# Optimization experiments

Measured on AMD Instinct MI355X. Metric: run time of the kernel, lower is better.

The kernel has to match this reference:

```python
import jax, jax.numpy as jnp
import numpy as np

B, M, T, L, K = 64, 16, 2048, 64, 32
N = T - L + 1  # 1985 sliding-window positions


def setup_inputs() -> dict:
    key = jax.random.key(0)
    k1, k2, k3 = jax.random.split(key, 3)
    x = jax.random.normal(k1, (B, M, T), dtype=jnp.float32)
    # shapelets initialized uniform(-1, 1) as in nn.init.uniform_
    shapelets = jax.random.uniform(k2, (K, L), dtype=jnp.float32, minval=-1.0, maxval=1.0)
    # penalty maps (learned; zeros at init, random here for a non-trivial weighting)
    penalty_maps = 0.1 * jax.random.normal(k3, (K, M, N), dtype=jnp.float32)
    return {"x": x, "shapelets": shapelets, "penalty_maps": penalty_maps}


def reference(x, shapelets, penalty_maps):
    # x: (B, M, T); shapelets: (K, L); penalty_maps: (K, M, N)
    Lw = shapelets.shape[1]
    n_pos = x.shape[2] - Lw + 1
    # sliding-window view: (B, M, N, L), equivalent to torch unfold(dim=2, size=L, step=1)
    idx = jnp.arange(n_pos)[:, None] + jnp.arange(Lw)[None, :]
    sub = x[:, :, idx]  # (B, M, N, L)

    def per_shapelet(args):
        shp, pmap = args  # (L,), (M, N)
        # raw squared L2 distance over window, per channel/position: (B, M, N)
        raw = jnp.sum((sub - shp[None, None, None, :]) ** 2, axis=3)
        pen = jax.nn.elu(-pmap) + 2.0  # (M, N)
        wd = jnp.sum(raw * pen[None], axis=1)  # sum over channels -> (B, N)
        return jnp.min(wd, axis=1)  # min over positions -> (B,)

    # sequential map over the K shapelets avoids a Kx blow-up of the (B,M,N,L) intermediate
    feats = jax.lax.map(per_shapelet, (shapelets, penalty_maps))  # (K, B)
    return feats.T  # (B, K)
```

## Files before the change

### kernel.cpp

```cpp
#include <hip/hip_runtime.h>
#include <hip/hip_bf16.h>

#define B_ 64
#define M_ 16
#define T_ 2048
#define L_ 64
#define K_ 32
#define N_ (T_ - L_ + 1)
#define TN 64
#define NT_ 32
#define NTH 256
#define XROW 144
#define STSTR 72
#define PENK (NT_ * M_ * 64)
#define PENSZ (K_ * PENK)

typedef __attribute__((ext_vector_type(8))) short bf16x8;
typedef __attribute__((ext_vector_type(4))) float f32x4;

__device__ __forceinline__ unsigned short f2bf(float f) {
    __hip_bfloat16 h = __float2bfloat16(f);
    return __builtin_bit_cast(unsigned short, h);
}

__device__ __forceinline__ float elu_pen(float p) {
    return (p < 0.f) ? (2.f - p) : (__expf(-p) + 1.f);
}

__global__ void pen_init_kernel(const float* __restrict__ pmap,
                                const float* __restrict__ shp,
                                float* __restrict__ pen,
                                float* __restrict__ ss_ws,
                                unsigned* __restrict__ out) {
    const int gid = blockIdx.x * 256 + threadIdx.x;
    if (gid < B_ * K_) out[gid] = 0x7F800000u;
    if (gid < K_) {
        float s = 0.f;
        for (int l = 0; l < L_; ++l) { float v = shp[gid * L_ + l]; s = fmaf(v, v, s); }
        ss_ws[gid] = s;
    }
    if (gid < PENSZ / 4) {
        const int o = gid * 4;
        const int nin = o & 63;
        const int m   = (o >> 6) & 15;
        const int nt  = (o >> 10) & 31;
        const int k   = o >> 15;
        const int n   = nt * TN + nin;
        const float* src = pmap + ((size_t)k * M_ + m) * N_ + n;
        float p[4];
        if (n + 3 < N_) {
            float4 v = *(const float4*)src;
            p[0] = v.x; p[1] = v.y; p[2] = v.z; p[3] = v.w;
        } else {
#pragma unroll
            for (int i = 0; i < 4; ++i) p[i] = (n + i < N_) ? src[i] : 0.f;
        }
        float4 r;
        r.x = elu_pen(p[0]); r.y = elu_pen(p[1]);
        r.z = elu_pen(p[2]); r.w = elu_pen(p[3]);
        *(float4*)(pen + o) = r;
    }
}

__global__ __launch_bounds__(NTH, 4)
void shapelet_mfma_kernel(const float* __restrict__ x,
                          const float* __restrict__ shp,
                          const float* __restrict__ pen,
                          const float* __restrict__ ss_ws,
                          unsigned* __restrict__ out) {
    __shared__ __align__(16) unsigned short xbuf4[M_][4][XROW];
    __shared__ __align__(16) unsigned short st[K_][STSTR];
    __shared__ __align__(16) float sqw[M_][TN];

    const int tid = threadIdx.x;
    const int bx = blockIdx.x;
    const int n0 = bx * TN;
    const int b  = blockIdx.y;
    const bool fast = (n0 + 2 * TN <= T_);

    const int lane = tid & 63;
    const int w  = tid >> 6;
    const int rl = lane & 15;
    const int q  = lane >> 4;
    const int sp = rl & 3;
    const int e0 = 16 * w + 8 * q + (rl & ~3);
    const int eq = e0 >> 2;
    const int nrow = n0 + 16 * w + 4 * q;

    const float ssk0 = ss_ws[rl], ssk1 = ss_ws[16 + rl];

    const float* pb0 = pen + (size_t)rl * PENK + (size_t)bx * (M_ * 64) + (16 * w + 4 * q);
    const float* pb1 = pb0 + (size_t)16 * PENK;

    float4 pa0 = *(const float4*)(pb0);
    float4 pa1 = *(const float4*)(pb1);
    float4 pc0 = *(const float4*)(pb0 + 64);
    float4 pc1 = *(const float4*)(pb1 + 64);

    if (tid < 128) {
        const int m = tid >> 3, j0 = (tid & 7) * 8;
        const float* xr = x + ((size_t)b * M_ + m) * T_ + n0;
        float s = 0.f;
        if (fast) {
#pragma unroll
            for (int qd = 0; qd < 16; ++qd) {
                float4 v = *(const float4*)(xr + j0 + qd * 4);
                s = fmaf(v.x, v.x, s); s = fmaf(v.y, v.y, s);
                s = fmaf(v.z, v.z, s); s = fmaf(v.w, v.w, s);
            }
            sqw[m][j0] = s;
#pragma unroll
            for (int d = 1; d < 8; ++d) {
                float a = xr[j0 + d + L_ - 1], r = xr[j0 + d - 1];
                s += a * a - r * r;
                sqw[m][j0 + d] = s;
            }
        } else {
            for (int l = 0; l < L_; ++l) {
                float v = (n0 + j0 + l < T_) ? xr[j0 + l] : 0.f;
                s = fmaf(v, v, s);
            }
            sqw[m][j0] = s;
            for (int d = 1; d < 8; ++d) {
                float a = (n0 + j0 + d + L_ - 1 < T_) ? xr[j0 + d + L_ - 1] : 0.f;
                float r = (n0 + j0 + d - 1 < T_) ? xr[j0 + d - 1] : 0.f;
                s += a * a - r * r;
                sqw[m][j0 + d] = s;
            }
        }
    } else {
        const int t2 = tid - 128;
        const float* xb = x + ((size_t)b * M_) * T_ + n0;
        for (int g = t2; g < M_ * 31; g += 128) {
            const int m = g / 31, j4 = (g - m * 31) * 4;
            const float* src = xb + m * T_ + j4;
            float h[8];
            if (fast) {
                float4 v0 = *(const float4*)src;
                float4 v1 = *(const float4*)(src + 4);
                h[0] = v0.x; h[1] = v0.y; h[2] = v0.z; h[3] = v0.w;
                h[4] = v1.x; h[5] = v1.y; h[6] = v1.z; h[7] = v1.w;
            } else {
#pragma unroll
                for (int i = 0; i < 8; ++i)
                    h[i] = (n0 + j4 + i < T_) ? src[i] : 0.f;
            }
            unsigned short hb[8];
#pragma unroll
            for (int i = 0; i < 8; ++i) hb[i] = f2bf(h[i]);
#pragma unroll
            for (int s = 0; s < 4; ++s) {
                ushort4 sv = { hb[s], hb[s + 1], hb[s + 2], hb[s + 3] };
                *(ushort4*)&xbuf4[m][s][j4] = sv;
            }
        }
        for (int i = t2; i < K_ * 16; i += 128) {
            const int k = i >> 4, l4 = (i & 15) * 4;
            float4 v = *(const float4*)(shp + k * L_ + l4);
            ushort4 sv = { f2bf(v.x), f2bf(v.y), f2bf(v.z), f2bf(v.w) };
            *(ushort4*)&st[k][l4] = sv;
        }
    }
    __syncthreads();

    bf16x8 bfr[2][2];
#pragma unroll
    for (int t = 0; t < 2; ++t)
#pragma unroll
        for (int h = 0; h < 2; ++h)
            bfr[t][h] = *(const bf16x8*)&st[16 * t + rl][8 * q + 32 * h];

    f32x4 wd0 = (f32x4)0.f, wd1 = (f32x4)0.f;
    const f32x4 zero = (f32x4)0.f;

    auto mstep = [&](int m, float4 pm0, float4 pm1) {
        const uint2* prow = (const uint2*)&xbuf4[m][sp][0];
        uint2 lo0 = prow[eq],     hi0 = prow[eq + 1];
        uint2 lo1 = prow[eq + 8], hi1 = prow[eq + 9];
        union { uint2 u2[2]; bf16x8 v; } fa0, fa1;
        fa0.u2[0] = lo0; fa0.u2[1] = hi0;
        fa1.u2[0] = lo1; fa1.u2[1] = hi1;

        f32x4 c0_ = __builtin_amdgcn_mfma_f32_16x16x32_bf16(fa0.v, bfr[0][0], zero, 0, 0, 0);
        c0_       = __builtin_amdgcn_mfma_f32_16x16x32_bf16(fa1.v, bfr[0][1], c0_, 0, 0, 0);
        f32x4 c1_ = __builtin_amdgcn_mfma_f32_16x16x32_bf16(fa0.v, bfr[1][0], zero, 0, 0, 0);
        c1_       = __builtin_amdgcn_mfma_f32_16x16x32_bf16(fa1.v, bfr[1][1], c1_, 0, 0, 0);

        const float pe0[4] = { pm0.x, pm0.y, pm0.z, pm0.w };
        const float pe1[4] = { pm1.x, pm1.y, pm1.z, pm1.w };
        f32x4 sq = *(const f32x4*)&sqw[m][16 * w + 4 * q];
#pragma unroll
        for (int r = 0; r < 4; ++r) {
            float u0 = fmaf(-2.f, c0_[r], sq[r] + ssk0);
            wd0[r] = fmaf(pe0[r], u0, wd0[r]);
            float u1 = fmaf(-2.f, c1_[r], sq[r] + ssk1);
            wd1[r] = fmaf(pe1[r], u1, wd1[r]);
        }
    };

    for (int mp = 0; mp < M_ / 2; ++mp) {
        const int m = 2 * mp;
        float4 c0 = pa0, c1 = pa1, d0 = pc0, d1 = pc1;
        if (mp + 1 < M_ / 2) {
            const float* q0 = pb0 + (size_t)(m + 2) * 64;
            const float* q1 = pb1 + (size_t)(m + 2) * 64;
            pa0 = *(const float4*)(q0);
            pa1 = *(const float4*)(q1);
            pc0 = *(const float4*)(q0 + 64);
            pc1 = *(const float4*)(q1 + 64);
        }
        mstep(m, c0, c1);
        mstep(m + 1, d0, d1);
    }

    __syncthreads();
    float* red = (float*)&sqw[0][0];
#pragma unroll
    for (int t = 0; t < 2; ++t) {
        float lmin = __int_as_float(0x7F800000);
        const f32x4 wdv = t ? wd1 : wd0;
#pragma unroll
        for (int r = 0; r < 4; ++r)
            if (nrow + r < N_) lmin = fminf(lmin, wdv[r]);
        lmin = fminf(lmin, __shfl_xor(lmin, 16));
        lmin = fminf(lmin, __shfl_xor(lmin, 32));
        if (q == 0) red[w * 32 + t * 16 + rl] = lmin;
    }
    __syncthreads();
    if (tid < K_) {
        float v = fminf(fminf(red[tid], red[32 + tid]),
                        fminf(red[64 + tid], red[96 + tid]));
        atomicMin(out + (size_t)b * K_ + tid, __float_as_uint(fmaxf(v, 0.f)));
    }
}

extern "C" void kernel_launch(void* const* d_in, const int* in_sizes, int n_in,
                              void* d_out, int out_size, void* d_ws, size_t ws_size,
                              hipStream_t stream) {
    const float* x    = (const float*)d_in[0];
    const float* shp  = (const float*)d_in[1];
    const float* pmap = (const float*)d_in[2];
    unsigned* out = (unsigned*)d_out;
    float* pen   = (float*)d_ws;
    float* ss_ws = pen + PENSZ;

    pen_init_kernel<<<dim3(PENSZ / 4 / 256), dim3(256), 0, stream>>>(
        pmap, shp, pen, ss_ws, out);

    dim3 grid(NT_, B_);
    shapelet_mfma_kernel<<<grid, dim3(NTH), 0, stream>>>(x, shp, pen, ss_ws, out);
}
```

Baseline: 117.2 us.

## Load shapelet fragments directly into registers, drop shared staging, raise occupancy

Shapelet bf16 MFMA fragments and their squared norms are now computed straight from global memory into registers, with a shuffle reduction, instead of staging through shared memory and a workspace. This removes the st shared buffer and the ss_ws precompute. All threads now share the x staging loop, and the penalty prefetch pipeline is replaced by a simple unroll-2 loop that loads per channel. Launch bounds go from 4 to 6 blocks per CU to raise occupancy, at the risk of register pressure and less explicit latency hiding for the penalty loads.

```diff
diff --git a/kernel.cpp b/kernel.cpp
--- a/kernel.cpp
+++ b/kernel.cpp
@@ -11,7 +11,6 @@
 #define NT_ 32
 #define NTH 256
 #define XROW 144
-#define STSTR 72
 #define PENK (NT_ * M_ * 64)
 #define PENSZ (K_ * PENK)
 
@@ -28,17 +27,10 @@
 }
 
 __global__ void pen_init_kernel(const float* __restrict__ pmap,
-                                const float* __restrict__ shp,
                                 float* __restrict__ pen,
-                                float* __restrict__ ss_ws,
                                 unsigned* __restrict__ out) {
     const int gid = blockIdx.x * 256 + threadIdx.x;
     if (gid < B_ * K_) out[gid] = 0x7F800000u;
-    if (gid < K_) {
-        float s = 0.f;
-        for (int l = 0; l < L_; ++l) { float v = shp[gid * L_ + l]; s = fmaf(v, v, s); }
-        ss_ws[gid] = s;
-    }
     if (gid < PENSZ / 4) {
         const int o = gid * 4;
         const int nin = o & 63;
@@ -62,14 +54,12 @@
     }
 }
 
-__global__ __launch_bounds__(NTH, 4)
+__global__ __launch_bounds__(NTH, 6)
 void shapelet_mfma_kernel(const float* __restrict__ x,
                           const float* __restrict__ shp,
                           const float* __restrict__ pen,
-                          const float* __restrict__ ss_ws,
                           unsigned* __restrict__ out) {
     __shared__ __align__(16) unsigned short xbuf4[M_][4][XROW];
-    __shared__ __align__(16) unsigned short st[K_][STSTR];
     __shared__ __align__(16) float sqw[M_][TN];
 
     const int tid = threadIdx.x;
@@ -77,6 +67,65 @@
     const int n0 = bx * TN;
     const int b  = blockIdx.y;
     const bool fast = (n0 + 2 * TN <= T_);
+
+    const float* xb = x + ((size_t)b * M_) * T_ + n0;
+    for (int g = tid; g < M_ * 31; g += NTH) {
+        const int m = g / 31, j4 = (g - m * 31) * 4;
+        const float* src = xb + m * T_ + j4;
+        float h[8];
+        if (fast) {
+            float4 v0 = *(const float4*)src;
+            float4 v1 = *(const float4*)(src + 4);
+            h[0] = v0.x; h[1] = v0.y; h[2] = v0.z; h[3] = v0.w;
+            h[4] = v1.x; h[5] = v1.y; h[6] = v1.z; h[7] = v1.w;
+        } else {
+#pragma unroll
+            for (int i = 0; i < 8; ++i)
+                h[i] = (n0 + j4 + i < T_) ? src[i] : 0.f;
+        }
+        unsigned short hb[8];
+#pragma unroll
+        for (int i = 0; i < 8; ++i) hb[i] = f2bf(h[i]);
+#pragma unroll
+        for (int s = 0; s < 4; ++s) {
+            ushort4 sv = { hb[s], hb[s + 1], hb[s + 2], hb[s + 3] };
+            *(ushort4*)&xbuf4[m][s][j4] = sv;
+        }
+    }
+    if (tid < M_ * 8) {
+        const int m = tid >> 3, j0 = (tid & 7) * 8;
+        const float* xr = x + ((size_t)b * M_ + m) * T_ + n0;
+        if (fast) {
+            float s0 = 0.f, s1 = 0.f, s2 = 0.f, s3 = 0.f;
+#pragma unroll
+            for (int qd = 0; qd < 16; ++qd) {
+                float4 v = *(const float4*)(xr + j0 + qd * 4);
+                s0 = fmaf(v.x, v.x, s0); s1 = fmaf(v.y, v.y, s1);
+                s2 = fmaf(v.z, v.z, s2); s3 = fmaf(v.w, v.w, s3);
+            }
+            float s = (s0 + s1) + (s2 + s3);
+            sqw[m][j0] = s;
+#pragma unroll
+            for (int d = 1; d < 8; ++d) {
+                float a = xr[j0 + d + L_ - 1], r = xr[j0 + d - 1];
+                s += a * a - r * r;
+                sqw[m][j0 + d] = s;
+            }
+        } else {
+            float s = 0.f;
+            for (int l = 0; l < L_; ++l) {
+                float v = (n0 + j0 + l < T_) ? xr[j0 + l] : 0.f;
+                s = fmaf(v, v, s);
+            }
+            sqw[m][j0] = s;
+            for (int d = 1; d < 8; ++d) {
+                float a = (n0 + j0 + d + L_ - 1 < T_) ? xr[j0 + d + L_ - 1] : 0.f;
+                float r = (n0 + j0 + d - 1 < T_) ? xr[j0 + d - 1] : 0.f;
+                s += a * a - r * r;
+                sqw[m][j0 + d] = s;
+            }
+        }
+    }
 
     const int lane = tid & 63;
     const int w  = tid >> 6;
@@ -87,93 +136,42 @@
     const int eq = e0 >> 2;
     const int nrow = n0 + 16 * w + 4 * q;
 
-    const float ssk0 = ss_ws[rl], ssk1 = ss_ws[16 + rl];
+    bf16x8 bfr[2][2];
+    float ssk0 = 0.f, ssk1 = 0.f;
+#pragma unroll
+    for (int t = 0; t < 2; ++t) {
+        float* ssp = t ? &ssk1 : &ssk0;
+#pragma unroll
+        for (int h = 0; h < 2; ++h) {
+            const float* sp_ = shp + (16 * t + rl) * L_ + 8 * q + 32 * h;
+            float4 a = *(const float4*)sp_;
+            float4 c = *(const float4*)(sp_ + 4);
+            *ssp = fmaf(a.x, a.x, *ssp); *ssp = fmaf(a.y, a.y, *ssp);
+            *ssp = fmaf(a.z, a.z, *ssp); *ssp = fmaf(a.w, a.w, *ssp);
+            *ssp = fmaf(c.x, c.x, *ssp); *ssp = fmaf(c.y, c.y, *ssp);
+            *ssp = fmaf(c.z, c.z, *ssp); *ssp = fmaf(c.w, c.w, *ssp);
+            bf16x8 f = { (short)f2bf(a.x), (short)f2bf(a.y), (short)f2bf(a.z),
+                         (short)f2bf(a.w), (short)f2bf(c.x), (short)f2bf(c.y),
+                         (short)f2bf(c.z), (short)f2bf(c.w) };
+            bfr[t][h] = f;
+        }
+    }
+    ssk0 += __shfl_xor(ssk0, 16); ssk0 += __shfl_xor(ssk0, 32);
+    ssk1 += __shfl_xor(ssk1, 16); ssk1 += __shfl_xor(ssk1, 32);
+
+    __syncthreads();
 
     const float* pb0 = pen + (size_t)rl * PENK + (size_t)bx * (M_ * 64) + (16 * w + 4 * q);
     const float* pb1 = pb0 + (size_t)16 * PENK;
 
-    float4 pa0 = *(const float4*)(pb0);
-    float4 pa1 = *(const float4*)(pb1);
-    float4 pc0 = *(const float4*)(pb0 + 64);
-    float4 pc1 = *(const float4*)(pb1 + 64);
-
-    if (tid < 128) {
-        const int m = tid >> 3, j0 = (tid & 7) * 8;
-        const float* xr = x + ((size_t)b * M_ + m) * T_ + n0;
-        float s = 0.f;
-        if (fast) {
-#pragma unroll
-            for (int qd = 0; qd < 16; ++qd) {
-                float4 v = *(const float4*)(xr + j0 + qd * 4);
-                s = fmaf(v.x, v.x, s); s = fmaf(v.y, v.y, s);
-                s = fmaf(v.z, v.z, s); s = fmaf(v.w, v.w, s);
-            }
-            sqw[m][j0] = s;
-#pragma unroll
-            for (int d = 1; d < 8; ++d) {
-                float a = xr[j0 + d + L_ - 1], r = xr[j0 + d - 1];
-                s += a * a - r * r;
-                sqw[m][j0 + d] = s;
-            }
-        } else {
-            for (int l = 0; l < L_; ++l) {
-                float v = (n0 + j0 + l < T_) ? xr[j0 + l] : 0.f;
-                s = fmaf(v, v, s);
-            }
-            sqw[m][j0] = s;
-            for (int d = 1; d < 8; ++d) {
-                float a = (n0 + j0 + d + L_ - 1 < T_) ? xr[j0 + d + L_ - 1] : 0.f;
-                float r = (n0 + j0 + d - 1 < T_) ? xr[j0 + d - 1] : 0.f;
-                s += a * a - r * r;
-                sqw[m][j0 + d] = s;
-            }
-        }
-    } else {
-        const int t2 = tid - 128;
-        const float* xb = x + ((size_t)b * M_) * T_ + n0;
-        for (int g = t2; g < M_ * 31; g += 128) {
-            const int m = g / 31, j4 = (g - m * 31) * 4;
-            const float* src = xb + m * T_ + j4;
-            float h[8];
-            if (fast) {
-                float4 v0 = *(const float4*)src;
-                float4 v1 = *(const float4*)(src + 4);
-                h[0] = v0.x; h[1] = v0.y; h[2] = v0.z; h[3] = v0.w;
-                h[4] = v1.x; h[5] = v1.y; h[6] = v1.z; h[7] = v1.w;
-            } else {
-#pragma unroll
-                for (int i = 0; i < 8; ++i)
-                    h[i] = (n0 + j4 + i < T_) ? src[i] : 0.f;
-            }
-            unsigned short hb[8];
-#pragma unroll
-            for (int i = 0; i < 8; ++i) hb[i] = f2bf(h[i]);
-#pragma unroll
-            for (int s = 0; s < 4; ++s) {
-                ushort4 sv = { hb[s], hb[s + 1], hb[s + 2], hb[s + 3] };
-                *(ushort4*)&xbuf4[m][s][j4] = sv;
-            }
-        }
-        for (int i = t2; i < K_ * 16; i += 128) {
-            const int k = i >> 4, l4 = (i & 15) * 4;
-            float4 v = *(const float4*)(shp + k * L_ + l4);
-            ushort4 sv = { f2bf(v.x), f2bf(v.y), f2bf(v.z), f2bf(v.w) };
-            *(ushort4*)&st[k][l4] = sv;
-        }
-    }
-    __syncthreads();
-
-    bf16x8 bfr[2][2];
-#pragma unroll
-    for (int t = 0; t < 2; ++t)
-#pragma unroll
-        for (int h = 0; h < 2; ++h)
-            bfr[t][h] = *(const bf16x8*)&st[16 * t + rl][8 * q + 32 * h];
-
     f32x4 wd0 = (f32x4)0.f, wd1 = (f32x4)0.f;
     const f32x4 zero = (f32x4)0.f;
 
-    auto mstep = [&](int m, float4 pm0, float4 pm1) {
+#pragma unroll 2
+    for (int m = 0; m < M_; ++m) {
+        float4 pm0 = *(const float4*)(pb0 + (size_t)m * 64);
+        float4 pm1 = *(const float4*)(pb1 + (size_t)m * 64);
+
         const uint2* prow = (const uint2*)&xbuf4[m][sp][0];
         uint2 lo0 = prow[eq],     hi0 = prow[eq + 1];
         uint2 lo1 = prow[eq + 8], hi1 = prow[eq + 9];
@@ -196,21 +194,6 @@
             float u1 = fmaf(-2.f, c1_[r], sq[r] + ssk1);
             wd1[r] = fmaf(pe1[r], u1, wd1[r]);
         }
-    };
-
-    for (int mp = 0; mp < M_ / 2; ++mp) {
-        const int m = 2 * mp;
-        float4 c0 = pa0, c1 = pa1, d0 = pc0, d1 = pc1;
-        if (mp + 1 < M_ / 2) {
-            const float* q0 = pb0 + (size_t)(m + 2) * 64;
-            const float* q1 = pb1 + (size_t)(m + 2) * 64;
-            pa0 = *(const float4*)(q0);
-            pa1 = *(const float4*)(q1);
-            pc0 = *(const float4*)(q0 + 64);
-            pc1 = *(const float4*)(q1 + 64);
-        }
-        mstep(m, c0, c1);
-        mstep(m + 1, d0, d1);
     }
 
     __syncthreads();
@@ -242,11 +225,9 @@
     const float* pmap = (const float*)d_in[2];
     unsigned* out = (unsigned*)d_out;
     float* pen   = (float*)d_ws;
-    float* ss_ws = pen + PENSZ;
-
-    pen_init_kernel<<<dim3(PENSZ / 4 / 256), dim3(256), 0, stream>>>(
-        pmap, shp, pen, ss_ws, out);
+
+    pen_init_kernel<<<dim3(PENSZ / 4 / 256), dim3(256), 0, stream>>>(pmap, pen, out);
 
     dim3 grid(NT_, B_);
-    shapelet_mfma_kernel<<<grid, dim3(NTH), 0, stream>>>(x, shp, pen, ss_ws, out);
-}
+    shapelet_mfma_kernel<<<grid, dim3(NTH), 0, stream>>>(x, shp, pen, out);
+}
```

New measurement: 130.9 us. 1.12x slower.
